# Kernel optimization log

Measured on AMD Instinct MI355X. Metric: run time of the kernel, lower is better.

## Reference

```python
import jax, jax.numpy as jnp
import numpy as np

LMAX = 6; MMAX = 2
C = 128          # num_channels
H = 8            # num_heads
ALPHA = 32       # attn_alpha_channels
VAL = 16         # attn_value_channels (H*VAL == C)
HID = 64         # attn_hidden_channels
FFN = 128        # ffn_hidden_channels
NL = 4           # num_layers
CUTOFF = 12.0; NRBF = 600
AVG_DEG = 23.395238876342773
AVG_NODES = 77.81317
EPS = 1e-16

def _maps():
    idx, ls = [], []
    for l in range(LMAX + 1):
        mm = min(l, MMAX)
        for m in range(-mm, mm + 1):
            idx.append(l * l + l + m); ls.append(l)
    return np.array(idx), np.array(ls)
_M2F_np, _LOF_np = _maps()
M2F = jnp.asarray(_M2F_np)   # [KM] full-coefficient index of each m-restricted coeff
LOF = jnp.asarray(_LOF_np)   # [KM] degree l of each m-restricted coeff
KM = int(_M2F_np.shape[0])   # 29 for lmax=6, mmax=2
KF = (LMAX + 1) ** 2         # 49

def _rbf(d):
    # GaussianSmearing(0, cutoff, NRBF, width_scalar=2.0)
    off = jnp.linspace(0.0, CUTOFF, NRBF)
    coeff = -0.5 / (2.0 * (off[1] - off[0])) ** 2
    return jnp.exp(coeff * (d[:, None] - off) ** 2)

def _envelope(d):
    # PolynomialEnvelope, exponent p=5
    x = d / CUTOFF
    env = 1.0 - 21.0 * x ** 5 + 35.0 * x ** 6 - 15.0 * x ** 7
    return jnp.where(x < 1.0, env, 0.0)

def _rms(x, g):
    # merge-norm over channel dim with learned per-channel scale
    return x * jax.lax.rsqrt(jnp.mean(x * x, axis=-1, keepdims=True) + 1e-6) * g

def _forward(atomic_numbers, edge_index, edge_distance, emb,
             We0, be0, We1, be1, Weproj, gamma1, gamma2,
             Wr0, Wr1, Wrl, Wmsg, Wap, wa, Wg, Wv, Wo,
             Wf1, Wfg, Wf2, Wh1, Wh2):
    N = atomic_numbers.shape[0]
    src, tgt = edge_index[0], edge_index[1]
    rbf = _rbf(edge_distance)            # [E, NRBF]
    env = _envelope(edge_distance)       # [E]
    # node init: atom embedding on the l=0 component
    x = jnp.zeros((N, KF, C), rbf.dtype).at[:, 0, :].set(emb[atomic_numbers])
    # edge-degree embedding: radial MLP -> per-edge coeffs -> scatter to targets
    h = jax.nn.silu(rbf @ We0 + be0)
    h = jax.nn.silu(h @ We1 + be1)
    deg = (h @ Weproj).reshape(-1, KM, C)              # [E, KM, C]
    x = x.at[tgt[:, None], M2F[None, :], :].add(deg / AVG_DEG)
    for i in range(NL):
        # ---- equivariant graph attention ----
        y = _rms(x, gamma1[i])
        ym = y[:, M2F, :]                               # [N, KM, C] m-restricted
        m = jnp.concatenate([ym[src], ym[tgt]], axis=-1)  # [E, KM, 2C]
        m = jnp.einsum('ekc,ch->ekh', m, Wmsg[i])       # [E, KM, HID]
        # radial function, shared across m within each l (use_rad_l_parametrization)
        rad = jax.nn.silu(jax.nn.silu(rbf @ Wr0[i]) @ Wr1[i])
        radl = rad @ Wrl[i]                             # [E, LMAX+1]
        m = m * radl[:, LOF][..., None]
        # attention logits from invariant (l=0) part
        a = jax.nn.silu(m[:, 0, :] @ Wap[i]).reshape(-1, H, ALPHA)
        logits = jnp.einsum('eha,ha->eh', a, wa[i])     # [E, H]
        segmax = jnp.full((N, H), -jnp.inf, logits.dtype).at[tgt].max(logits)
        ex = env[:, None] * jnp.exp(logits - segmax[tgt])  # envelope-masked softmax
        den = jax.ops.segment_sum(ex, tgt, num_segments=N)
        attn = ex / (den[tgt] + EPS)                    # [E, H]
        # SwiGLU-gated equivariant values
        g = jax.nn.silu(m[:, 0, :] @ Wg[i])             # [E, H*VAL]
        v = jnp.einsum('ekh,hv->ekv', m, Wv[i]) * g[:, None, :]
        v = v.reshape(-1, KM, H, VAL) * attn[:, None, :, None]
        agg = jax.ops.segment_sum(v.reshape(-1, KM, H * VAL), tgt, num_segments=N)
        out = jnp.einsum('nkv,vc->nkc', agg, Wo[i])     # [N, KM, C]
        x = x.at[:, M2F, :].add(out)
        # ---- feed-forward (grid-MLP style SwiGLU) ----
        y = _rms(x, gamma2[i])
        gf = jax.nn.silu(y[:, 0, :] @ Wfg[i])           # [N, FFN]
        hf = jnp.einsum('nkc,cf->nkf', y, Wf1[i]) * gf[:, None, :]
        x = x + jnp.einsum('nkf,fc->nkc', hf, Wf2[i])
    # energy head on invariant part, sum-aggregated over nodes
    s = jax.nn.silu(x[:, 0, :] @ Wh1) @ Wh2             # [N, 1]
    return (jnp.sum(s) / AVG_NODES).reshape(1)

def setup_inputs() -> dict:
    key = jax.random.key(0)
    ks = jax.random.split(key, 24)
    N, E = 6000, 120000
    def rn(k, shape, scale=0.05):
        return jax.random.normal(k, shape, dtype=jnp.float32) * scale
    inp = {}
    inp['atomic_numbers'] = jax.random.randint(ks[0], (N,), 0, 128)
    inp['edge_index'] = jax.random.randint(ks[1], (2, E), 0, N)
    inp['edge_distance'] = jax.random.uniform(ks[2], (E,), minval=0.5, maxval=CUTOFF, dtype=jnp.float32)
    inp['emb'] = rn(ks[3], (128, C), 1.0)
    inp['We0'] = rn(ks[4], (NRBF, 128)); inp['be0'] = jnp.zeros((128,), jnp.float32)
    inp['We1'] = rn(ks[5], (128, 128)); inp['be1'] = jnp.zeros((128,), jnp.float32)
    inp['Weproj'] = rn(ks[6], (128, KM * C))
    inp['gamma1'] = jnp.ones((NL, C), jnp.float32)
    inp['gamma2'] = jnp.ones((NL, C), jnp.float32)
    inp['Wr0'] = rn(ks[7], (NL, NRBF, 128))
    inp['Wr1'] = rn(ks[8], (NL, 128, 128))
    inp['Wrl'] = rn(ks[9], (NL, 128, LMAX + 1), 0.1)
    inp['Wmsg'] = rn(ks[10], (NL, 2 * C, HID))
    inp['Wap'] = rn(ks[11], (NL, HID, H * ALPHA))
    inp['wa'] = rn(ks[12], (NL, H, ALPHA))
    inp['Wg'] = rn(ks[13], (NL, HID, H * VAL))
    inp['Wv'] = rn(ks[14], (NL, HID, H * VAL))
    inp['Wo'] = rn(ks[15], (NL, H * VAL, C))
    inp['Wf1'] = rn(ks[16], (NL, C, FFN))
    inp['Wfg'] = rn(ks[17], (NL, C, FFN))
    inp['Wf2'] = rn(ks[18], (NL, FFN, C))
    inp['Wh1'] = rn(ks[19], (C, C))
    inp['Wh2'] = rn(ks[20], (C, 1))
    return inp

def reference(atomic_numbers, edge_index, edge_distance, emb,
              We0, be0, We1, be1, Weproj, gamma1, gamma2,
              Wr0, Wr1, Wrl, Wmsg, Wap, wa, Wg, Wv, Wo,
              Wf1, Wfg, Wf2, Wh1, Wh2):
    return _forward(atomic_numbers, edge_index, edge_distance, emb,
                    We0, be0, We1, be1, Weproj, gamma1, gamma2,
                    Wr0, Wr1, Wrl, Wmsg, Wap, wa, Wg, Wv, Wo,
                    Wf1, Wfg, Wf2, Wh1, Wh2)
```

## Files before the change

kernel.cpp:

```cpp
#include <hip/hip_runtime.h>

#define KM 29
#define GTAB 2048

typedef __bf16 bf16_t;
typedef __bf16 bf16x8 __attribute__((ext_vector_type(8)));
typedef __bf16 bf16x4 __attribute__((ext_vector_type(4)));
typedef __bf16 bf16x2 __attribute__((ext_vector_type(2)));
typedef float  f32x4  __attribute__((ext_vector_type(4)));
typedef float  f32x2  __attribute__((ext_vector_type(2)));

__device__ __forceinline__ float silu_f(float x){ return x / (1.0f + __expf(-x)); }

__device__ __forceinline__ float wave_reduce_sum(float v){
  #pragma unroll
  for (int s = 1; s < 64; s <<= 1) v += __shfl_xor(v, s);
  return v;
}

__device__ __forceinline__ constexpr int LOF2(int k){
  return (k<1)?0 : (k<4)?1 : (k<9)?2 : (k<14)?3 : (k<19)?4 : (k<24)?5 : 6;
}

__device__ __forceinline__ f32x4 mfma16(bf16x8 a, bf16x8 b, f32x4 c){
  return __builtin_amdgcn_mfma_f32_16x16x32_bf16(a, b, c, 0, 0, 0);
}

__device__ __forceinline__ float env_f(float d){
  float xx = d*(1.0f/12.0f);
  float x2 = xx*xx, x4 = x2*x2, x5 = x4*xx;
  float env = 1.0f - 21.0f*x5 + 35.0f*x5*xx - 15.0f*x5*x2;
  return (xx < 1.0f) ? env : 0.0f;
}

__global__ void k_count(const int* __restrict__ EI, int* __restrict__ cnt, int E){
  int e = blockIdx.x*256 + threadIdx.x;
  if (e < E) atomicAdd(&cnt[EI[E+e]], 1);
}

__global__ __launch_bounds__(1024) void k_scan(int* __restrict__ cnt, int* __restrict__ rowptr, int N){
  __shared__ int ts[1024];
  int t = threadIdx.x;
  int base = t*8;
  int loc[8]; int sum = 0;
  #pragma unroll
  for (int u = 0; u < 8; u++){ int idx = base+u; int v = (idx < N) ? cnt[idx] : 0; loc[u] = sum; sum += v; }
  ts[t] = sum; __syncthreads();
  for (int off = 1; off < 1024; off <<= 1){
    int v = (t >= off) ? ts[t-off] : 0;
    __syncthreads();
    ts[t] += v;
    __syncthreads();
  }
  int excl = ts[t] - sum;
  #pragma unroll
  for (int u = 0; u < 8; u++){
    int idx = base+u;
    if (idx < N){ int r = excl + loc[u]; rowptr[idx] = r; cnt[idx] = r; }
  }
  if (t == 1023) rowptr[N] = ts[1023];
}

__global__ void k_fill(const int* __restrict__ EI, int* __restrict__ cur, int* __restrict__ order, int E){
  int e = blockIdx.x*256 + threadIdx.x;
  if (e < E){ int pos = atomicAdd(&cur[EI[E+e]], 1); order[pos] = e; }
}

__global__ void k_sort(const int* __restrict__ rowptr, int* __restrict__ order, int N){
  int n = blockIdx.x*256 + threadIdx.x;
  if (n >= N) return;
  int rp = rowptr[n], re = rowptr[n+1];
  for (int a = rp+1; a < re; a++){
    int key = order[a]; int b = a-1;
    while (b >= rp && order[b] > key){ order[b+1] = order[b]; b--; }
    order[b+1] = key;
  }
}

__global__ void k_tr(const float* __restrict__ src, bf16_t* __restrict__ dst,
                     int L, int R, int C, int Lstr){
  int idx = blockIdx.x*256 + threadIdx.x;
  int total = L*R*C;
  if (idx >= total) return;
  int l = idx / (R*C); int rem = idx - l*(R*C);
  int r = rem / C; int c = rem - r*C;
  dst[((size_t)l*C + c)*R + r] = (bf16_t)src[(size_t)l*Lstr + (size_t)r*C + c];
}

__global__ void k_tr2(const float* __restrict__ src, bf16_t* __restrict__ dst){
  int idx = blockIdx.x*256 + threadIdx.x;
  if (idx >= 4*128*128) return;
  int l = idx >> 14; int j = (idx >> 7) & 127; int c = idx & 127;
  float v = (j < 64) ? src[(size_t)l*16384 + c*64 + j]
                     : src[(size_t)l*16384 + 8192 + c*64 + (j-64)];
  dst[idx] = (bf16_t)v;
}

__global__ __launch_bounds__(256) void k_tab_embed(
    const float* __restrict__ We0, const float* __restrict__ be0,
    const float* __restrict__ We1, const float* __restrict__ be1,
    const float* __restrict__ Wr0, const float* __restrict__ Wr1, const float* __restrict__ Wrl,
    float* __restrict__ h2tab, float* __restrict__ radtab)
{
  __shared__ float sb[4][640];
  const int wid = threadIdx.x >> 6, lane = threadIdx.x & 63;
  const int e = blockIdx.x*4 + wid;
  if (e >= GTAB) return;
  const float d = e * (12.0f/(GTAB-1));
  const float DLT = 12.0f/599.0f;
  const float CO  = -0.5f/((2.0f*DLT)*(2.0f*DLT));
  int jc = (int)(d/DLT + 0.5f);
  int j0 = jc - 16; if (j0 < 0) j0 = 0; if (j0 > 600-32) j0 = 600-32;
  float diff = d - (float)(j0+lane)*DLT;
  float gval = __expf(CO*diff*diff);
  float p[10];
  #pragma unroll
  for (int u = 0; u < 10; u++) p[u] = 0.f;
  const int c2 = 2*lane;
  for (int jj = 0; jj < 32; jj++){
    float gj = __shfl(gval, jj);
    int row = j0 + jj;
    const float2 w0 = *(const float2*)(We0 + row*128 + c2);
    p[0] += gj*w0.x; p[1] += gj*w0.y;
    #pragma unroll
    for (int i = 0; i < 4; i++){
      const float2 wr = *(const float2*)(Wr0 + ((size_t)i*600 + row)*128 + c2);
      p[2+2*i] += gj*wr.x; p[3+2*i] += gj*wr.y;
    }
  }
  sb[wid][c2]   = silu_f(p[0] + be0[c2]);
  sb[wid][c2+1] = silu_f(p[1] + be0[c2+1]);
  #pragma unroll
  for (int i = 0; i < 4; i++){
    sb[wid][128 + 128*i + c2]   = silu_f(p[2+2*i]);
    sb[wid][128 + 128*i + c2+1] = silu_f(p[3+2*i]);
  }
  float a0 = 0.f, a1 = 0.f;
  for (int c = 0; c < 128; c++){
    float hv = sb[wid][c];
    const float2 w = *(const float2*)(We1 + c*128 + c2);
    a0 += hv*w.x; a1 += hv*w.y;
  }
  a0 = silu_f(a0 + be1[c2]); a1 = silu_f(a1 + be1[c2+1]);
  h2tab[(size_t)e*128 + c2]     = a0;
  h2tab[(size_t)e*128 + c2 + 1] = a1;
  #pragma unroll
  for (int i = 0; i < 4; i++){
    float r0 = 0.f, r1 = 0.f;
    const float* W1 = Wr1 + (size_t)i*128*128;
    for (int c = 0; c < 128; c++){
      float rv = sb[wid][128 + 128*i + c];
      const float2 w = *(const float2*)(W1 + c*128 + c2);
      r0 += rv*w.x; r1 += rv*w.y;
    }
    r0 = silu_f(r0); r1 = silu_f(r1);
    const float* Wl = Wrl + (size_t)i*128*7;
    float pl[7];
    #pragma unroll
    for (int l = 0; l < 7; l++) pl[l] = r0*Wl[c2*7+l] + r1*Wl[(c2+1)*7+l];
    #pragma unroll
    for (int l = 0; l < 7; l++) pl[l] = wave_reduce_sum(pl[l]);
    if (lane == 0){
      #pragma unroll
      for (int l = 0; l < 7; l++) radtab[(size_t)e*28 + i*7 + l] = pl[l];
    }
  }
}

__global__ void k_h2e(const float* __restrict__ ed, const float* __restrict__ h2tab,
                      bf16_t* __restrict__ h2e, int E){
  int idx = blockIdx.x*256 + threadIdx.x;
  if (idx >= E*128) return;
  int e = idx >> 7, ch = idx & 127;
  float d = ed[e];
  float u = d * ((GTAB-1)/12.0f);
  int j = (int)u; if (j > GTAB-2) j = GTAB-2;
  float f = u - (float)j;
  float a = h2tab[(size_t)j*128 + ch], b = h2tab[(size_t)(j+1)*128 + ch];
  h2e[idx] = (bf16_t)(a + f*(b-a));
}

__global__ __launch_bounds__(256) void k_h2sum(
    const bf16_t* __restrict__ h2e, const int* __restrict__ rowptr, const int* __restrict__ order,
    bf16_t* __restrict__ h2sum, int N)
{
  int n = blockIdx.x*2 + (threadIdx.x >> 7);
  int ch = threadIdx.x & 127;
  if (n >= N) return;
  int rp = rowptr[n], deg = rowptr[n+1] - rp;
  float acc = 0.f;
  for (int idx = 0; idx < deg; idx++){
    int e = order[rp+idx];
    acc += (float)h2e[(size_t)e*128 + ch];
  }
  h2sum[(size_t)n*128 + ch] = (bf16_t)acc;
}

__global__ __launch_bounds__(256) void k_init_x(
    const int* __restrict__ Z, const float* __restrict__ emb,
    const bf16_t* __restrict__ WeprojT, const bf16_t* __restrict__ h2sum,
    bf16_t* __restrict__ Xb, int N)
{
  __shared__ bf16_t h2s[32*136];
  __shared__ int Zs[32];
  int n0 = blockIdx.x*32, t = threadIdx.x;
  for (int idx = t; idx < 32*128; idx += 256){
    int nn = idx >> 7, ch = idx & 127;
    int n = n0 + nn;
    h2s[nn*136 + ch] = (n < N) ? h2sum[(size_t)n*128 + ch] : (bf16_t)0.f;
  }
  if (t < 32) Zs[t] = (n0 + t < N) ? Z[n0+t] : 0;
  __syncthreads();
  int wid = t >> 6, lane = t & 63;
  int mtile = wid & 1;
  int row = mtile*16 + (lane & 15);
  int koff = (lane >> 4)*8;
  bf16x8 afr[4];
  #pragma unroll
  for (int kk = 0; kk < 4; kk++) afr[kk] = *(const bf16x8*)(h2s + row*136 + kk*32 + koff);
  for (int nt = (wid>>1); nt < 232; nt += 2){
    f32x4 acc = {0.f,0.f,0.f,0.f};
    int col = nt*16 + (lane & 15);
    #pragma unroll
    for (int kk = 0; kk < 4; kk++){
      bf16x8 b = *(const bf16x8*)(WeprojT + (size_t)col*128 + kk*32 + koff);
      acc = mfma16(afr[kk], b, acc);
    }
    #pragma unroll
    for (int r = 0; r < 4; r++){
      int r32 = mtile*16 + (lane>>4)*4 + r;
      int n = n0 + r32;
      if (n < N){
        float v = acc[r] * (1.0f/23.395238876342773f);
        if (col < 128) v += emb[(size_t)Zs[r32]*128 + col];
        Xb[(size_t)n*3712 + col] = (bf16_t)v;
      }
    }
  }
}

__global__ __launch_bounds__(512) void k_pqv(
    const bf16_t* __restrict__ Xb, const float* __restrict__ gamma1,
    const bf16_t* __restrict__ WmsgCT, const bf16_t* __restrict__ WvT,
    unsigned char* __restrict__ PV8, unsigned char* __restrict__ QV8,
    float* __restrict__ P0, float* __restrict__ Q0, int layer)
{
  __shared__ bf16_t ys16[32*136];
  __shared__ bf16_t pq16[32*136];
  int n = blockIdx.x, t = threadIdx.x;
  int wid = t >> 6, lane = t & 63;
  const float* g1 = gamma1 + layer*128;
  const bf16_t* xp = Xb + (size_t)n*3712;
  for (int k = wid; k < KM; k += 8){
    float x0 = (float)xp[k*128 + lane], x1 = (float)xp[k*128 + 64 + lane];
    float ss = wave_reduce_sum(x0*x0 + x1*x1);
    float sc = rsqrtf(ss*(1.0f/128.0f) + 1e-6f);
    ys16[k*136 + lane]      = (bf16_t)(x0*sc*g1[lane]);
    ys16[k*136 + 64 + lane] = (bf16_t)(x1*sc*g1[64+lane]);
  }
  for (int idx = t; idx < 3*136; idx += 512) ys16[29*136 + idx] = (bf16_t)0.f;
  __syncthreads();
  int mtile = wid >> 2;
  int row = mtile*16 + (lane & 15);
  int koff = (lane >> 4)*8;
  {
    const bf16_t* Bc = WmsgCT + (size_t)layer*16384;
    f32x4 acc[2] = {{0,0,0,0},{0,0,0,0}};
    #pragma unroll
    for (int kk = 0; kk < 128; kk += 32){
      bf16x8 a = *(const bf16x8*)(ys16 + row*136 + kk + koff);
      #pragma unroll
      for (int u = 0; u < 2; u++){
        int col = ((wid&3)*2+u)*16 + (lane & 15);
        bf16x8 b = *(const bf16x8*)(Bc + (size_t)col*128 + kk + koff);
        acc[u] = mfma16(a, b, acc[u]);
      }
    }
    #pragma unroll
    for (int u = 0; u < 2; u++){
      int col = ((wid&3)*2+u)*16 + (lane & 15);
      #pragma unroll
      for (int r = 0; r < 4; r++){
        int r32 = mtile*16 + (lane>>4)*4 + r;
        pq16[r32*136 + col] = (bf16_t)acc[u][r];
      }
      if (mtile == 0 && (lane>>4) == 0){
        float v = acc[u][0];
        if (col < 64) P0[(size_t)n*64 + col] = v;
        else          Q0[(size_t)n*64 + col - 64] = v;
      }
    }
  }
  __syncthreads();
  {
    const bf16_t* Bt = WvT + (size_t)layer*8192;
    f32x4 acc[2] = {{0,0,0,0},{0,0,0,0}};
    #pragma unroll
    for (int kk = 0; kk < 64; kk += 32){
      bf16x8 a = *(const bf16x8*)(pq16 + row*136 + kk + koff);
      #pragma unroll
      for (int u = 0; u < 2; u++){
        int col = ((wid&3)*2+u)*16 + (lane & 15);
        bf16x8 b = *(const bf16x8*)(Bt + (size_t)col*64 + kk + koff);
        acc[u] = mfma16(a, b, acc[u]);
      }
    }
    unsigned char* pvp = PV8 + (size_t)n*4096;
    int r0i = mtile*16 + (lane>>4)*4;
    #pragma unroll
    for (int u = 0; u < 2; u++){
      int col = ((wid&3)*2+u)*16 + (lane & 15);
      float pk[4];
      #pragma unroll
      for (int r = 0; r < 4; r++){
        int r32 = r0i + r;
        pk[r] = (r32 < KM) ? acc[u][r] : 0.f;
      }
      int dw = __builtin_amdgcn_cvt_pk_fp8_f32(pk[0], pk[1], 0, false);
      dw = __builtin_amdgcn_cvt_pk_fp8_f32(pk[2], pk[3], dw, true);
      *(unsigned int*)(pvp + col*32 + r0i) = (unsigned int)dw;
    }
  }
  {
    const bf16_t* Bt = WvT + (size_t)layer*8192;
    f32x4 acc[2] = {{0,0,0,0},{0,0,0,0}};
    #pragma unroll
    for (int kk = 0; kk < 64; kk += 32){
      bf16x8 a = *(const bf16x8*)(pq16 + row*136 + 64 + kk + koff);
      #pragma unroll
      for (int u = 0; u < 2; u++){
        int col = ((wid&3)*2+u)*16 + (lane & 15);
        bf16x8 b = *(const bf16x8*)(Bt + (size_t)col*64 + kk + koff);
        acc[u] = mfma16(a, b, acc[u]);
      }
    }
    unsigned char* qvp = QV8 + (size_t)n*4096;
    int r0i = mtile*16 + (lane>>4)*4;
    #pragma unroll
    for (int u = 0; u < 2; u++){
      int col = ((wid&3)*2+u)*16 + (lane & 15);
      float pk[4];
      #pragma unroll
      for (int r = 0; r < 4; r++){
        int r32 = r0i + r;
        pk[r] = (r32 < KM) ? acc[u][r] : 0.f;
      }
      int dw = __builtin_amdgcn_cvt_pk_fp8_f32(pk[0], pk[1], 0, false);
      dw = __builtin_amdgcn_cvt_pk_fp8_f32(pk[2], pk[3], dw, true);
      *(unsigned int*)(qvp + col*32 + r0i) = (unsigned int)dw;
    }
  }
}

__global__ __launch_bounds__(256) void k_edge_logits(
    const int* __restrict__ EI, const float* __restrict__ ed,
    const float* __restrict__ P0, const float* __restrict__ Q0,
    const float* __restrict__ radtab, const bf16_t* __restrict__ WapT, const float* __restrict__ wa,
    const bf16_t* __restrict__ WgT, float* __restrict__ logi, bf16_t* __restrict__ gate16,
    int E, int layer)
{
  __shared__ bf16_t m0s[16*72];
  __shared__ int   srcs[16], tgts[16];
  __shared__ float r0s[16];
  int t = threadIdx.x;
  int eb = blockIdx.x*16;
  if (t < 16){
    int e = eb + t;
    if (e < E){
      srcs[t] = EI[e]; tgts[t] = EI[E+e];
      float d = ed[e];
      float u = d * ((GTAB-1)/12.0f);
      int j = (int)u; if (j > GTAB-2) j = GTAB-2;
      float f = u - (float)j;
      float a = radtab[(size_t)j*28 + layer*7], b = radtab[(size_t)(j+1)*28 + layer*7];
      r0s[t] = a + f*(b-a);
    } else { srcs[t] = 0; tgts[t] = 0; r0s[t] = 0.f; }
  }
  __syncthreads();
  #pragma unroll
  for (int u = 0; u < 4; u++){
    int idx = t + u*256;
    int i = idx >> 6, j = idx & 63;
    m0s[i*72 + j] = (bf16_t)((P0[(size_t)srcs[i]*64 + j] + Q0[(size_t)tgts[i]*64 + j]) * r0s[i]);
  }
  __syncthreads();
  int wid = t >> 6, lane = t & 63;
  int l15 = lane & 15, lg = lane >> 4;
  int koff = lg*8;
  bf16x8 a0 = *(const bf16x8*)(m0s + l15*72 + koff);
  bf16x8 a1 = *(const bf16x8*)(m0s + l15*72 + 32 + koff);
  const bf16_t* Ba = WapT + (size_t)layer*16384;
  const bf16_t* Bg = WgT  + (size_t)layer*8192;
  const float* wav = wa + layer*256;
  f32x4 accA[4], accG[2];
  #pragma unroll
  for (int u = 0; u < 4; u++){
    int col = 64*wid + u*16 + l15;
    f32x4 acc = {0,0,0,0};
    acc = mfma16(a0, *(const bf16x8*)(Ba + (size_t)col*64 + koff), acc);
    acc = mfma16(a1, *(const bf16x8*)(Ba + (size_t)col*64 + 32 + koff), acc);
    accA[u] = acc;
  }
  #pragma unroll
  for (int u = 0; u < 2; u++){
    int col = 32*wid + u*16 + l15;
    f32x4 acc = {0,0,0,0};
    acc = mfma16(a0, *(const bf16x8*)(Bg + (size_t)col*64 + koff), acc);
    acc = mfma16(a1, *(const bf16x8*)(Bg + (size_t)col*64 + 32 + koff), acc);
    accG[u] = acc;
  }
  #pragma unroll
  for (int u = 0; u < 2; u++){
    int col = 32*wid + u*16 + l15;
    #pragma unroll
    for (int r = 0; r < 4; r++){
      int e = eb + lg*4 + r;
      if (e < E) gate16[(size_t)e*128 + col] = (bf16_t)silu_f(accG[u][r]);
    }
  }
  #pragma unroll
  for (int hpair = 0; hpair < 2; hpair++){
    int c0 = 64*wid + hpair*32 + l15;
    float w0 = wav[c0], w1 = wav[c0+16];
    float s[4];
    #pragma unroll
    for (int r = 0; r < 4; r++)
      s[r] = silu_f(accA[2*hpair][r])*w0 + silu_f(accA[2*hpair+1][r])*w1;
    #pragma unroll
    for (int r = 0; r < 4; r++){
      s[r] += __shfl_xor(s[r], 1);
      s[r] += __shfl_xor(s[r], 2);
      s[r] += __shfl_xor(s[r], 4);
      s[r] += __shfl_xor(s[r], 8);
    }
    if (l15 == 0){
      #pragma unroll
      for (int r = 0; r < 4; r++){
        int e = eb + lg*4 + r;
        if (e < E) logi[(size_t)e*8 + 2*wid + hpair] = s[r];
      }
    }
  }
}

#define FMA_DW(dw, kb) { \
  f32x2 lo_ = __builtin_amdgcn_cvt_pk_f32_fp8((dw), false); \
  f32x2 hi_ = __builtin_amdgcn_cvt_pk_f32_fp8((dw), true); \
  acc[(kb)]   += lo_.x * rw[LOF2((kb))]; \
  acc[(kb)+1] += lo_.y * rw[LOF2((kb)+1)]; \
  acc[(kb)+2] += hi_.x * rw[LOF2((kb)+2)]; \
  acc[(kb)+3] += hi_.y * rw[LOF2((kb)+3)]; }

__global__ __launch_bounds__(512, 4) void k_gather(
    const int* __restrict__ EI, const int* __restrict__ rowptr, const int* __restrict__ order,
    const float* __restrict__ ed,
    const unsigned char* __restrict__ PV8, const unsigned char* __restrict__ QV8,
    const bf16_t* __restrict__ gate16, const float* __restrict__ logi,
    const float* __restrict__ radtab,
    bf16_t* __restrict__ agg, int layer)
{
  __shared__ bf16_t mA[32*136];
  __shared__ bf16_t mB[32*136];
  __shared__ float at8[512];
  __shared__ float rl7[512];
  __shared__ int   esb[64], srcs[64];
  __shared__ float denl[32];

  int n = blockIdx.x, t = threadIdx.x;
  int rp = rowptr[n], deg = rowptr[n+1] - rp;
  if (deg == 0){
    for (int idx = t; idx < 3712; idx += 512) agg[(size_t)n*3712 + idx] = (bf16_t)0.f;
    return;
  }
  int eg = t >> 7, hv = t & 127, h = hv >> 4;
  float acc[32];
  #pragma unroll
  for (int j = 0; j < 32; j++) acc[j] = 0.f;
  float S[7];
  #pragma unroll
  for (int l = 0; l < 7; l++) S[l] = 0.f;
  float dpart = 0.f;
  for (int base = 0; base < deg; base += 64){
    int ne = min(64, deg - base);
    if (base > 0) __syncthreads();
    if (t < ne){ int e = order[rp + base + t]; esb[t] = e; srcs[t] = EI[e]; }
    __syncthreads();
    if (t < ne*8){
      int i = t >> 3, q = t & 7;
      int e = esb[i];
      float d = ed[e];
      at8[t] = env_f(d) * __expf(logi[(size_t)e*8 + q]);
      if (q < 7){
        float u = d * ((GTAB-1)/12.0f);
        int j = (int)u; if (j > GTAB-2) j = GTAB-2;
        float f = u - (float)j;
        float a = radtab[(size_t)j*28 + layer*7 + q], b = radtab[(size_t)(j+1)*28 + layer*7 + q];
        rl7[t] = a + f*(b-a);
      }
    }
    __syncthreads();
    uint4 A0 = {0,0,0,0}, A1 = {0,0,0,0}, B0 = {0,0,0,0}, B1 = {0,0,0,0};
    float gA = 0.f, gB = 0.f;
    int i = eg;
    if (i < ne){
      const uint4* p = (const uint4*)(PV8 + (size_t)srcs[i]*4096 + hv*32);
      A0 = p[0]; A1 = p[1];
      gA = (float)gate16[(size_t)esb[i]*128 + hv];
    }
    if (i + 4 < ne){
      const uint4* p = (const uint4*)(PV8 + (size_t)srcs[i+4]*4096 + hv*32);
      B0 = p[0]; B1 = p[1];
      gB = (float)gate16[(size_t)esb[i+4]*128 + hv];
    }
    while (i < ne){
      int i2 = i + 8;
      uint4 C0 = {0,0,0,0}, C1 = {0,0,0,0}; float gC = 0.f;
      if (i2 < ne){
        const uint4* p = (const uint4*)(PV8 + (size_t)srcs[i2]*4096 + hv*32);
        C0 = p[0]; C1 = p[1];
        gC = (float)gate16[(size_t)esb[i2]*128 + hv];
      }
      float ae = at8[i*8 + h];
      dpart += ae;
      float w = gA * ae;
      float rw[7];
      #pragma unroll
      for (int l = 0; l < 7; l++){ rw[l] = rl7[i*8 + l]*w; S[l] += rw[l]; }
      FMA_DW(A0.x, 0)  FMA_DW(A0.y, 4)  FMA_DW(A0.z, 8)  FMA_DW(A0.w, 12)
      FMA_DW(A1.x, 16) FMA_DW(A1.y, 20) FMA_DW(A1.z, 24) FMA_DW(A1.w, 28)
      A0 = B0; A1 = B1; gA = gB;
      B0 = C0; B1 = C1; gB = gC;
      i += 4;
    }
  }
  {
    const unsigned char* qvp = QV8 + (size_t)n*4096 + hv*32;
    uint4 q0 = *(const uint4*)qvp;
    uint4 q1 = *(const uint4*)(qvp + 16);
    float rw[7];
    #pragma unroll
    for (int l = 0; l < 7; l++) rw[l] = S[l];
    FMA_DW(q0.x, 0)  FMA_DW(q0.y, 4)  FMA_DW(q0.z, 8)  FMA_DW(q0.w, 12)
    FMA_DW(q1.x, 16) FMA_DW(q1.y, 20) FMA_DW(q1.z, 24) FMA_DW(q1.w, 28)
  }
  if ((hv & 15) == 0) denl[eg*8 + h] = dpart;
  __syncthreads();
  {
    float dsum = denl[h] + denl[8 + h] + denl[16 + h] + denl[24 + h];
    float inv = 1.0f/(dsum + 1e-30f);
    #pragma unroll
    for (int j = 0; j < 32; j++) acc[j] *= inv;
  }
  if (eg == 0){
    #pragma unroll
    for (int j = 0; j < 32; j++) mA[j*136 + hv] = (bf16_t)acc[j];
  } else if (eg == 1){
    #pragma unroll
    for (int j = 0; j < 32; j++) mB[j*136 + hv] = (bf16_t)acc[j];
  }
  __syncthreads();
  if (eg == 2){
    #pragma unroll
    for (int j = 0; j < 32; j++) mA[j*136 + hv] = (bf16_t)((float)mA[j*136 + hv] + acc[j]);
  } else if (eg == 3){
    #pragma unroll
    for (int j = 0; j < 32; j++) mB[j*136 + hv] = (bf16_t)((float)mB[j*136 + hv] + acc[j]);
  }
  __syncthreads();
  for (int idx = t; idx < 3712; idx += 512){
    int k = idx >> 7, c = idx & 127;
    agg[(size_t)n*3712 + idx] = (bf16_t)((float)mA[k*136 + c] + (float)mB[k*136 + c]);
  }
}

__global__ __launch_bounds__(512, 4) void k_xupdate(
    const bf16_t* __restrict__ agg,
    const float* __restrict__ gamma1, const float* __restrict__ gamma2,
    const float* __restrict__ Wfg,
    const bf16_t* __restrict__ Wf1T, const bf16_t* __restrict__ Wf2T,
    const bf16_t* __restrict__ WoT, const bf16_t* __restrict__ WmsgCT, const bf16_t* __restrict__ WvT,
    bf16_t* __restrict__ Xb, int layer,
    unsigned char* __restrict__ PV8o, unsigned char* __restrict__ QV8o,
    float* __restrict__ P0o, float* __restrict__ Q0o, int do_tail)
{
  __shared__ float  xs[3712];
  __shared__ bf16_t ysag[32*136];
  __shared__ bf16_t hsqv[32*136];
  __shared__ float  pf[640];

  int n = blockIdx.x, t = threadIdx.x;
  int wid = t >> 6, lane = t & 63;

  {
    const bf16x2* Xp2 = (const bf16x2*)(Xb + (size_t)n*3712);
    for (int p = t; p < 1856; p += 512){
      bf16x2 v = Xp2[p];
      xs[2*p]   = (float)v.x;
      xs[2*p+1] = (float)v.y;
    }
  }
  for (int idx = t; idx < 3712; idx += 512){
    int k = idx >> 7, c = idx & 127;
    ysag[k*136 + c] = agg[(size_t)n*3712 + idx];
  }
  for (int idx = t; idx < 3*136; idx += 512) ysag[29*136 + idx] = (bf16_t)0.f;
  __syncthreads();
  {
    const bf16_t* Bt = WoT + (size_t)layer*16384;
    int mtile = wid >> 2, colt = (wid & 3)*2;
    int row = mtile*16 + (lane & 15);
    int koff = (lane >> 4)*8;
    f32x4 a2[2] = {{0,0,0,0},{0,0,0,0}};
    #pragma unroll
    for (int kk = 0; kk < 128; kk += 32){
      bf16x8 a = *(const bf16x8*)(ysag + row*136 + kk + koff);
      #pragma unroll
      for (int u = 0; u < 2; u++){
        int col = (colt+u)*16 + (lane & 15);
        bf16x8 b = *(const bf16x8*)(Bt + (size_t)col*128 + kk + koff);
        a2[u] = mfma16(a, b, a2[u]);
      }
    }
    #pragma unroll
    for (int u = 0; u < 2; u++){
      int col = (colt+u)*16 + (lane & 15);
      #pragma unroll
      for (int r = 0; r < 4; r++){
        int r32 = mtile*16 + (lane>>4)*4 + r;
        if (r32 < KM) xs[r32*128 + col] += a2[u][r];
      }
    }
  }
  __syncthreads();
  const float* g2 = gamma2 + layer*128;
  for (int k = wid; k < KM; k += 8){
    float x0 = xs[k*128 + lane], x1 = xs[k*128 + 64 + lane];
    float ss = wave_reduce_sum(x0*x0 + x1*x1);
    float sc = rsqrtf(ss*(1.0f/128.0f) + 1e-6f);
    ysag[k*136 + lane]      = (bf16_t)(x0*sc*g2[lane]);
    ysag[k*136 + 64 + lane] = (bf16_t)(x1*sc*g2[64+lane]);
  }
  for (int idx = t; idx < 3*136; idx += 512) ysag[29*136 + idx] = (bf16_t)0.f;
  __syncthreads();
  {
    int part = t >> 7, f = t & 127;
    const float* Wfgp = Wfg + (size_t)layer*16384;
    float p = 0.f;
    for (int c = part*32; c < part*32 + 32; c++) p += (float)ysag[c] * Wfgp[c*128 + f];
    pf[part*128 + f] = p;
  }
  __syncthreads();
  if (t < 128) pf[512 + t] = silu_f(pf[t] + pf[128+t] + pf[256+t] + pf[384+t]);
  __syncthreads();
  {
    const bf16_t* Bt = Wf1T + (size_t)layer*16384;
    int mtile = wid >> 2, colt = (wid & 3)*2;
    int row = mtile*16 + (lane & 15);
    int koff = (lane >> 4)*8;
    f32x4 a2[2] = {{0,0,0,0},{0,0,0,0}};
    #pragma unroll
    for (int kk = 0; kk < 128; kk += 32){
      bf16x8 a = *(const bf16x8*)(ysag + row*136 + kk + koff);
      #pragma unroll
      for (int u = 0; u < 2; u++){
        int col = (colt+u)*16 + (lane & 15);
        bf16x8 b = *(const bf16x8*)(Bt + (size_t)col*128 + kk + koff);
        a2[u] = mfma16(a, b, a2[u]);
      }
    }
    #pragma unroll
    for (int u = 0; u < 2; u++){
      int col = (colt+u)*16 + (lane & 15);
      float gfc = pf[512 + col];
      #pragma unroll
      for (int r = 0; r < 4; r++){
        int r32 = mtile*16 + (lane>>4)*4 + r;
        hsqv[r32*136 + col] = (bf16_t)(a2[u][r]*gfc);
      }
    }
  }
  __syncthreads();
  {
    const bf16_t* Bt = Wf2T + (size_t)layer*16384;
    int mtile = wid >> 2, colt = (wid & 3)*2;
    int row = mtile*16 + (lane & 15);
    int koff = (lane >> 4)*8;
    f32x4 a2[2] = {{0,0,0,0},{0,0,0,0}};
    #pragma unroll
    for (int kk = 0; kk < 128; kk += 32){
      bf16x8 a = *(const bf16x8*)(hsqv + row*136 + kk + koff);
      #pragma unroll
      for (int u = 0; u < 2; u++){
        int col = (colt+u)*16 + (lane & 15);
        bf16x8 b = *(const bf16x8*)(Bt + (size_t)col*128 + kk + koff);
        a2[u] = mfma16(a, b, a2[u]);
      }
    }
    #pragma unroll
    for (int u = 0; u < 2; u++){
      int col = (colt+u)*16 + (lane & 15);
      #pragma unroll
      for (int r = 0; r < 4; r++){
        int r32 = mtile*16 + (lane>>4)*4 + r;
        if (r32 < KM) xs[r32*128 + col] += a2[u][r];
      }
    }
  }
  __syncthreads();
  {
    bf16x2* Xp2 = (bf16x2*)(Xb + (size_t)n*3712);
    for (int p = t; p < 1856; p += 512){
      bf16x2 v;
      v.x = (bf16_t)xs[2*p];
      v.y = (bf16_t)xs[2*p+1];
      Xp2[p] = v;
    }
  }
  if (do_tail){
    const float* g1n = gamma1 + (size_t)(layer+1)*128;
    for (int k = wid; k < KM; k += 8){
      float x0 = xs[k*128 + lane], x1 = xs[k*128 + 64 + lane];
      float ss = wave_reduce_sum(x0*x0 + x1*x1);
      float sc = rsqrtf(ss*(1.0f/128.0f) + 1e-6f);
      ysag[k*136 + lane]      = (bf16_t)(x0*sc*g1n[lane]);
      ysag[k*136 + 64 + lane] = (bf16_t)(x1*sc*g1n[64+lane]);
    }
    __syncthreads();
    int mtile = wid >> 2;
    int row = mtile*16 + (lane & 15);
    int koff = (lane >> 4)*8;
    {
      const bf16_t* Bc = WmsgCT + (size_t)(layer+1)*16384;
      f32x4 acc[2] = {{0,0,0,0},{0,0,0,0}};
      #pragma unroll
      for (int kk = 0; kk < 128; kk += 32){
        bf16x8 a = *(const bf16x8*)(ysag + row*136 + kk + koff);
        #pragma unroll
        for (int u = 0; u < 2; u++){
          int col = ((wid&3)*2+u)*16 + (lane & 15);
          bf16x8 b = *(const bf16x8*)(Bc + (size_t)col*128 + kk + koff);
          acc[u] = mfma16(a, b, acc[u]);
        }
      }
      #pragma unroll
      for (int u = 0; u < 2; u++){
        int col = ((wid&3)*2+u)*16 + (lane & 15);
        #pragma unroll
        for (int r = 0; r < 4; r++){
          int r32 = mtile*16 + (lane>>4)*4 + r;
          hsqv[r32*136 + col] = (bf16_t)acc[u][r];
        }
        if (mtile == 0 && (lane>>4) == 0){
          float v = acc[u][0];
          if (col < 64) P0o[(size_t)n*64 + col] = v;
          else          Q0o[(size_t)n*64 + col - 64] = v;
        }
      }
    }
    __syncthreads();
    {
      const bf16_t* Bt = WvT + (size_t)(layer+1)*8192;
      f32x4 acc[2] = {{0,0,0,0},{0,0,0,0}};
      #pragma unroll
      for (int kk = 0; kk < 64; kk += 32){
        bf16x8 a = *(const bf16x8*)(hsqv + row*136 + kk + koff);
        #pragma unroll
        for (int u = 0; u < 2; u++){
          int col = ((wid&3)*2+u)*16 + (lane & 15);
          bf16x8 b = *(const bf16x8*)(Bt + (size_t)col*64 + kk + koff);
          acc[u] = mfma16(a, b, acc[u]);
        }
      }
      unsigned char* pvp = PV8o + (size_t)n*4096;
      int r0i = mtile*16 + (lane>>4)*4;
      #pragma unroll
      for (int u = 0; u < 2; u++){
        int col = ((wid&3)*2+u)*16 + (lane & 15);
        float pk[4];
        #pragma unroll
        for (int r = 0; r < 4; r++){
          int r32 = r0i + r;
          pk[r] = (r32 < KM) ? acc[u][r] : 0.f;
        }
        int dw = __builtin_amdgcn_cvt_pk_fp8_f32(pk[0], pk[1], 0, false);
        dw = __builtin_amdgcn_cvt_pk_fp8_f32(pk[2], pk[3], dw, true);
        *(unsigned int*)(pvp + col*32 + r0i) = (unsigned int)dw;
      }
    }
    {
      const bf16_t* Bt = WvT + (size_t)(layer+1)*8192;
      f32x4 acc[2] = {{0,0,0,0},{0,0,0,0}};
      #pragma unroll
      for (int kk = 0; kk < 64; kk += 32){
        bf16x8 a = *(const bf16x8*)(hsqv + row*136 + 64 + kk + koff);
        #pragma unroll
        for (int u = 0; u < 2; u++){
          int col = ((wid&3)*2+u)*16 + (lane & 15);
          bf16x8 b = *(const bf16x8*)(Bt + (size_t)col*64 + kk + koff);
          acc[u] = mfma16(a, b, acc[u]);
        }
      }
      unsigned char* qvp = QV8o + (size_t)n*4096;
      int r0i = mtile*16 + (lane>>4)*4;
      #pragma unroll
      for (int u = 0; u < 2; u++){
        int col = ((wid&3)*2+u)*16 + (lane & 15);
        float pk[4];
        #pragma unroll
        for (int r = 0; r < 4; r++){
          int r32 = r0i + r;
          pk[r] = (r32 < KM) ? acc[u][r] : 0.f;
        }
        int dw = __builtin_amdgcn_cvt_pk_fp8_f32(pk[0], pk[1], 0, false);
        dw = __builtin_amdgcn_cvt_pk_fp8_f32(pk[2], pk[3], dw, true);
        *(unsigned int*)(qvp + col*32 + r0i) = (unsigned int)dw;
      }
    }
  }
}

__global__ __launch_bounds__(256) void k_head(
    const bf16_t* __restrict__ Xb, const float* __restrict__ Wh1, const float* __restrict__ Wh2,
    float* __restrict__ partial, int N)
{
  __shared__ float wsum[4];
  int t = threadIdx.x;
  int half = t >> 7;
  int n = blockIdx.x*2 + half;
  int f = t & 127;
  float sv = 0.f;
  if (n < N){
    const bf16_t* xp = Xb + (size_t)n*3712;
    float acc = 0.f;
    for (int c = 0; c < 128; c++) acc += (float)xp[c]*Wh1[c*128 + f];
    sv = silu_f(acc)*Wh2[f];
  }
  sv = wave_reduce_sum(sv);
  if ((t & 63) == 0) wsum[t >> 6] = sv;
  __syncthreads();
  if (t == 0) partial[blockIdx.x] = wsum[0] + wsum[1] + wsum[2] + wsum[3];
}

__global__ __launch_bounds__(256) void k_reduce(const float* __restrict__ partial, float* __restrict__ out, int P){
  __shared__ float sh[256];
  int t = threadIdx.x;
  float s = 0.f;
  for (int i = t; i < P; i += 256) s += partial[i];
  sh[t] = s; __syncthreads();
  for (int off = 128; off > 0; off >>= 1){
    if (t < off) sh[t] += sh[t+off];
    __syncthreads();
  }
  if (t == 0) out[0] = sh[0] / 77.81317f;
}

extern "C" void kernel_launch(void* const* d_in, const int* in_sizes, int n_in,
                              void* d_out, int out_size, void* d_ws, size_t ws_size,
                              hipStream_t stream)
{
  const int*   Z      = (const int*)d_in[0];
  const int*   EI     = (const int*)d_in[1];
  const float* ed     = (const float*)d_in[2];
  const float* emb    = (const float*)d_in[3];
  const float* We0    = (const float*)d_in[4];
  const float* be0    = (const float*)d_in[5];
  const float* We1    = (const float*)d_in[6];
  const float* be1    = (const float*)d_in[7];
  const float* Weproj = (const float*)d_in[8];
  const float* gamma1 = (const float*)d_in[9];
  const float* gamma2 = (const float*)d_in[10];
  const float* Wr0    = (const float*)d_in[11];
  const float* Wr1    = (const float*)d_in[12];
  const float* Wrl    = (const float*)d_in[13];
  const float* Wmsg   = (const float*)d_in[14];
  const float* Wap    = (const float*)d_in[15];
  const float* wa     = (const float*)d_in[16];
  const float* Wg     = (const float*)d_in[17];
  const float* Wv     = (const float*)d_in[18];
  const float* Wo     = (const float*)d_in[19];
  const float* Wf1    = (const float*)d_in[20];
  const float* Wfg    = (const float*)d_in[21];
  const float* Wf2    = (const float*)d_in[22];
  const float* Wh1    = (const float*)d_in[23];
  const float* Wh2    = (const float*)d_in[24];

  const int N = in_sizes[0];
  const int E = in_sizes[2];

  float* ws = (float*)d_ws;
  size_t o = 0;
  auto alloc = [&](size_t nf){ float* p = ws + o; o += (nf + 7) & ~(size_t)7; return p; };

  bf16_t* Xb    = (bf16_t*)alloc((size_t)N*1856);
  float* P0     = alloc((size_t)N*64);
  float* Q0     = alloc((size_t)N*64);
  float* logi   = alloc((size_t)E*8);
  float* part   = alloc((size_t)((N+1)/2) + 8);
  float* radtab = alloc((size_t)GTAB*28);
  float* h2tab  = alloc((size_t)GTAB*128);
  bf16_t* h2sum = (bf16_t*)alloc((size_t)N*64);
  unsigned char* PV8 = (unsigned char*)alloc((size_t)N*1024);
  unsigned char* QV8 = (unsigned char*)alloc((size_t)N*1024);
  bf16_t* agg   = (bf16_t*)alloc((size_t)N*1856);
  bf16_t* gate16= (bf16_t*)alloc((size_t)E*64);
  bf16_t* arena = (bf16_t*)alloc(434176);
  int* rowptr = (int*)alloc((size_t)N+8);
  int* curs   = (int*)alloc((size_t)N);
  int* order  = (int*)alloc((size_t)E);

  bf16_t* WmsgCT  = arena;
  bf16_t* WvT     = arena + 65536;
  bf16_t* WoT     = arena + 98304;
  bf16_t* Wf1T    = arena + 163840;
  bf16_t* Wf2T    = arena + 229376;
  bf16_t* WapT    = arena + 294912;
  bf16_t* WgT     = arena + 360448;
  bf16_t* WeprojT = arena + 393216;

  bf16_t* h2e = gate16;

  hipMemsetAsync(curs, 0, sizeof(int)*N, stream);
  k_count<<<(E+255)/256, 256, 0, stream>>>(EI, curs, E);
  k_scan<<<1, 1024, 0, stream>>>(curs, rowptr, N);
  k_fill<<<(E+255)/256, 256, 0, stream>>>(EI, curs, order, E);
  k_sort<<<(N+255)/256, 256, 0, stream>>>(rowptr, order, N);

  k_tr2<<<256, 256, 0, stream>>>(Wmsg, WmsgCT);
  k_tr<<<128, 256, 0, stream>>>(Wv,   WvT,  4, 64, 128, 8192);
  k_tr<<<256, 256, 0, stream>>>(Wo,   WoT,  4, 128, 128, 16384);
  k_tr<<<256, 256, 0, stream>>>(Wf1,  Wf1T, 4, 128, 128, 16384);
  k_tr<<<256, 256, 0, stream>>>(Wf2,  Wf2T, 4, 128, 128, 16384);
  k_tr<<<256, 256, 0, stream>>>(Wap,  WapT, 4, 64, 256, 16384);
  k_tr<<<128, 256, 0, stream>>>(Wg,   WgT,  4, 64, 128, 8192);
  k_tr<<<1856, 256, 0, stream>>>(Weproj, WeprojT, 1, 128, 3712, 0);

  k_tab_embed<<<GTAB/4, 256, 0, stream>>>(We0, be0, We1, be1, Wr0, Wr1, Wrl, h2tab, radtab);
  k_h2e<<<(E*128+255)/256, 256, 0, stream>>>(ed, h2tab, h2e, E);
  k_h2sum<<<(N+1)/2, 256, 0, stream>>>(h2e, rowptr, order, h2sum, N);
  k_init_x<<<(N+31)/32, 256, 0, stream>>>(Z, emb, WeprojT, h2sum, Xb, N);

  k_pqv<<<N, 512, 0, stream>>>(Xb, gamma1, WmsgCT, WvT, PV8, QV8, P0, Q0, 0);

  for (int i = 0; i < 4; i++){
    k_edge_logits<<<(E+15)/16, 256, 0, stream>>>(EI, ed, P0, Q0, radtab, WapT, wa, WgT, logi, gate16, E, i);
    k_gather<<<N, 512, 0, stream>>>(EI, rowptr, order, ed, PV8, QV8, gate16, logi, radtab, agg, i);
    k_xupdate<<<N, 512, 0, stream>>>(agg, gamma1, gamma2, Wfg, Wf1T, Wf2T, WoT, WmsgCT, WvT,
                                     Xb, i, PV8, QV8, P0, Q0, (i < 3) ? 1 : 0);
  }

  int PB = (N+1)/2;
  k_head<<<PB, 256, 0, stream>>>(Xb, Wh1, Wh2, part, N);
  k_reduce<<<1, 256, 0, stream>>>(part, (float*)d_out, PB);
}
```

Baseline: 2.078 ms.

## Fuse h2e into h2sum, precompute edge attention/radial terms, persistent gather/update grids

Drops the separate k_h2e kernel and does the table interpolation inside k_h2sum, so the per-edge buffer is no longer written and then re-read. k_edge_logits now computes env*exp(logit) and all seven interpolated radial weights per edge and stores them, which lets k_gather just load them. k_gather and k_xupdate become grid-stride loops over a fixed grid of 1024 blocks instead of one block per node. The P/Q value MFMAs are merged into one loop that shares B-operand loads. The trade-offs are an extra E*7 float buffer, and the persistent grid may load-balance worse when node degrees vary.

New measurement: 2.721 ms. +30.9%, slower.

```diff
diff --git a/kernel.cpp b/kernel.cpp
--- a/kernel.cpp
+++ b/kernel.cpp
@@ -167,21 +167,9 @@
   }
 }
 
-__global__ void k_h2e(const float* __restrict__ ed, const float* __restrict__ h2tab,
-                      bf16_t* __restrict__ h2e, int E){
-  int idx = blockIdx.x*256 + threadIdx.x;
-  if (idx >= E*128) return;
-  int e = idx >> 7, ch = idx & 127;
-  float d = ed[e];
-  float u = d * ((GTAB-1)/12.0f);
-  int j = (int)u; if (j > GTAB-2) j = GTAB-2;
-  float f = u - (float)j;
-  float a = h2tab[(size_t)j*128 + ch], b = h2tab[(size_t)(j+1)*128 + ch];
-  h2e[idx] = (bf16_t)(a + f*(b-a));
-}
-
 __global__ __launch_bounds__(256) void k_h2sum(
-    const bf16_t* __restrict__ h2e, const int* __restrict__ rowptr, const int* __restrict__ order,
+    const float* __restrict__ ed, const float* __restrict__ h2tab,
+    const int* __restrict__ rowptr, const int* __restrict__ order,
     bf16_t* __restrict__ h2sum, int N)
 {
   int n = blockIdx.x*2 + (threadIdx.x >> 7);
@@ -191,7 +179,12 @@
   float acc = 0.f;
   for (int idx = 0; idx < deg; idx++){
     int e = order[rp+idx];
-    acc += (float)h2e[(size_t)e*128 + ch];
+    float d = ed[e];
+    float u = d * ((GTAB-1)/12.0f);
+    int j = (int)u; if (j > GTAB-2) j = GTAB-2;
+    float f = u - (float)j;
+    float a = h2tab[(size_t)j*128 + ch], b = h2tab[(size_t)(j+1)*128 + ch];
+    acc += a + f*(b-a);
   }
   h2sum[(size_t)n*128 + ch] = (bf16_t)acc;
 }
@@ -294,60 +287,39 @@
   __syncthreads();
   {
     const bf16_t* Bt = WvT + (size_t)layer*8192;
-    f32x4 acc[2] = {{0,0,0,0},{0,0,0,0}};
+    f32x4 accP[2] = {{0,0,0,0},{0,0,0,0}};
+    f32x4 accQ[2] = {{0,0,0,0},{0,0,0,0}};
     #pragma unroll
     for (int kk = 0; kk < 64; kk += 32){
-      bf16x8 a = *(const bf16x8*)(pq16 + row*136 + kk + koff);
+      bf16x8 aP = *(const bf16x8*)(pq16 + row*136 + kk + koff);
+      bf16x8 aQ = *(const bf16x8*)(pq16 + row*136 + 64 + kk + koff);
       #pragma unroll
       for (int u = 0; u < 2; u++){
         int col = ((wid&3)*2+u)*16 + (lane & 15);
         bf16x8 b = *(const bf16x8*)(Bt + (size_t)col*64 + kk + koff);
-        acc[u] = mfma16(a, b, acc[u]);
+        accP[u] = mfma16(aP, b, accP[u]);
+        accQ[u] = mfma16(aQ, b, accQ[u]);
       }
     }
     unsigned char* pvp = PV8 + (size_t)n*4096;
+    unsigned char* qvp = QV8 + (size_t)n*4096;
     int r0i = mtile*16 + (lane>>4)*4;
     #pragma unroll
     for (int u = 0; u < 2; u++){
       int col = ((wid&3)*2+u)*16 + (lane & 15);
-      float pk[4];
+      float pk[4], qk[4];
       #pragma unroll
       for (int r = 0; r < 4; r++){
         int r32 = r0i + r;
-        pk[r] = (r32 < KM) ? acc[u][r] : 0.f;
+        pk[r] = (r32 < KM) ? accP[u][r] : 0.f;
+        qk[r] = (r32 < KM) ? accQ[u][r] : 0.f;
       }
       int dw = __builtin_amdgcn_cvt_pk_fp8_f32(pk[0], pk[1], 0, false);
       dw = __builtin_amdgcn_cvt_pk_fp8_f32(pk[2], pk[3], dw, true);
       *(unsigned int*)(pvp + col*32 + r0i) = (unsigned int)dw;
-    }
-  }
-  {
-    const bf16_t* Bt = WvT + (size_t)layer*8192;
-    f32x4 acc[2] = {{0,0,0,0},{0,0,0,0}};
-    #pragma unroll
-    for (int kk = 0; kk < 64; kk += 32){
-      bf16x8 a = *(const bf16x8*)(pq16 + row*136 + 64 + kk + koff);
-      #pragma unroll
-      for (int u = 0; u < 2; u++){
-        int col = ((wid&3)*2+u)*16 + (lane & 15);
-        bf16x8 b = *(const bf16x8*)(Bt + (size_t)col*64 + kk + koff);
-        acc[u] = mfma16(a, b, acc[u]);
-      }
-    }
-    unsigned char* qvp = QV8 + (size_t)n*4096;
-    int r0i = mtile*16 + (lane>>4)*4;
-    #pragma unroll
-    for (int u = 0; u < 2; u++){
-      int col = ((wid&3)*2+u)*16 + (lane & 15);
-      float pk[4];
-      #pragma unroll
-      for (int r = 0; r < 4; r++){
-        int r32 = r0i + r;
-        pk[r] = (r32 < KM) ? acc[u][r] : 0.f;
-      }
-      int dw = __builtin_amdgcn_cvt_pk_fp8_f32(pk[0], pk[1], 0, false);
-      dw = __builtin_amdgcn_cvt_pk_fp8_f32(pk[2], pk[3], dw, true);
-      *(unsigned int*)(qvp + col*32 + r0i) = (unsigned int)dw;
+      int dw2 = __builtin_amdgcn_cvt_pk_fp8_f32(qk[0], qk[1], 0, false);
+      dw2 = __builtin_amdgcn_cvt_pk_fp8_f32(qk[2], qk[3], dw2, true);
+      *(unsigned int*)(qvp + col*32 + r0i) = (unsigned int)dw2;
     }
   }
 }
@@ -356,12 +328,13 @@
     const int* __restrict__ EI, const float* __restrict__ ed,
     const float* __restrict__ P0, const float* __restrict__ Q0,
     const float* __restrict__ radtab, const bf16_t* __restrict__ WapT, const float* __restrict__ wa,
-    const bf16_t* __restrict__ WgT, float* __restrict__ logi, bf16_t* __restrict__ gate16,
-    int E, int layer)
+    const bf16_t* __restrict__ WgT, float* __restrict__ expat, float* __restrict__ radl,
+    bf16_t* __restrict__ gate16, int E, int layer)
 {
   __shared__ bf16_t m0s[16*72];
   __shared__ int   srcs[16], tgts[16];
   __shared__ float r0s[16];
+  __shared__ float envs[16];
   int t = threadIdx.x;
   int eb = blockIdx.x*16;
   if (t < 16){
@@ -369,12 +342,18 @@
     if (e < E){
       srcs[t] = EI[e]; tgts[t] = EI[E+e];
       float d = ed[e];
+      envs[t] = env_f(d);
       float u = d * ((GTAB-1)/12.0f);
       int j = (int)u; if (j > GTAB-2) j = GTAB-2;
       float f = u - (float)j;
-      float a = radtab[(size_t)j*28 + layer*7], b = radtab[(size_t)(j+1)*28 + layer*7];
-      r0s[t] = a + f*(b-a);
-    } else { srcs[t] = 0; tgts[t] = 0; r0s[t] = 0.f; }
+      #pragma unroll
+      for (int l = 0; l < 7; l++){
+        float a = radtab[(size_t)j*28 + layer*7 + l], b = radtab[(size_t)(j+1)*28 + layer*7 + l];
+        float rv = a + f*(b-a);
+        radl[(size_t)e*7 + l] = rv;
+        if (l == 0) r0s[t] = rv;
+      }
+    } else { srcs[t] = 0; tgts[t] = 0; r0s[t] = 0.f; envs[t] = 0.f; }
   }
   __syncthreads();
   #pragma unroll
@@ -437,7 +416,7 @@
       #pragma unroll
       for (int r = 0; r < 4; r++){
         int e = eb + lg*4 + r;
-        if (e < E) logi[(size_t)e*8 + 2*wid + hpair] = s[r];
+        if (e < E) expat[(size_t)e*8 + 2*wid + hpair] = envs[lg*4 + r] * __expf(s[r]);
       }
     }
   }
@@ -453,11 +432,10 @@
 
 __global__ __launch_bounds__(512, 4) void k_gather(
     const int* __restrict__ EI, const int* __restrict__ rowptr, const int* __restrict__ order,
-    const float* __restrict__ ed,
     const unsigned char* __restrict__ PV8, const unsigned char* __restrict__ QV8,
-    const bf16_t* __restrict__ gate16, const float* __restrict__ logi,
-    const float* __restrict__ radtab,
-    bf16_t* __restrict__ agg, int layer)
+    const bf16_t* __restrict__ gate16, const float* __restrict__ expat,
+    const float* __restrict__ radl,
+    bf16_t* __restrict__ agg, int N)
 {
   __shared__ bf16_t mA[32*136];
   __shared__ bf16_t mB[32*136];
@@ -466,110 +444,107 @@
   __shared__ int   esb[64], srcs[64];
   __shared__ float denl[32];
 
-  int n = blockIdx.x, t = threadIdx.x;
-  int rp = rowptr[n], deg = rowptr[n+1] - rp;
-  if (deg == 0){
-    for (int idx = t; idx < 3712; idx += 512) agg[(size_t)n*3712 + idx] = (bf16_t)0.f;
-    return;
-  }
+  int t = threadIdx.x;
   int eg = t >> 7, hv = t & 127, h = hv >> 4;
-  float acc[32];
-  #pragma unroll
-  for (int j = 0; j < 32; j++) acc[j] = 0.f;
-  float S[7];
-  #pragma unroll
-  for (int l = 0; l < 7; l++) S[l] = 0.f;
-  float dpart = 0.f;
-  for (int base = 0; base < deg; base += 64){
-    int ne = min(64, deg - base);
-    if (base > 0) __syncthreads();
-    if (t < ne){ int e = order[rp + base + t]; esb[t] = e; srcs[t] = EI[e]; }
-    __syncthreads();
-    if (t < ne*8){
-      int i = t >> 3, q = t & 7;
-      int e = esb[i];
-      float d = ed[e];
-      at8[t] = env_f(d) * __expf(logi[(size_t)e*8 + q]);
-      if (q < 7){
-        float u = d * ((GTAB-1)/12.0f);
-        int j = (int)u; if (j > GTAB-2) j = GTAB-2;
-        float f = u - (float)j;
-        float a = radtab[(size_t)j*28 + layer*7 + q], b = radtab[(size_t)(j+1)*28 + layer*7 + q];
-        rl7[t] = a + f*(b-a);
-      }
-    }
-    __syncthreads();
-    uint4 A0 = {0,0,0,0}, A1 = {0,0,0,0}, B0 = {0,0,0,0}, B1 = {0,0,0,0};
-    float gA = 0.f, gB = 0.f;
-    int i = eg;
-    if (i < ne){
-      const uint4* p = (const uint4*)(PV8 + (size_t)srcs[i]*4096 + hv*32);
-      A0 = p[0]; A1 = p[1];
-      gA = (float)gate16[(size_t)esb[i]*128 + hv];
-    }
-    if (i + 4 < ne){
-      const uint4* p = (const uint4*)(PV8 + (size_t)srcs[i+4]*4096 + hv*32);
-      B0 = p[0]; B1 = p[1];
-      gB = (float)gate16[(size_t)esb[i+4]*128 + hv];
-    }
-    while (i < ne){
-      int i2 = i + 8;
-      uint4 C0 = {0,0,0,0}, C1 = {0,0,0,0}; float gC = 0.f;
-      if (i2 < ne){
-        const uint4* p = (const uint4*)(PV8 + (size_t)srcs[i2]*4096 + hv*32);
-        C0 = p[0]; C1 = p[1];
-        gC = (float)gate16[(size_t)esb[i2]*128 + hv];
-      }
-      float ae = at8[i*8 + h];
-      dpart += ae;
-      float w = gA * ae;
+
+  for (int n = blockIdx.x; n < N; n += gridDim.x){
+    int rp = rowptr[n], deg = rowptr[n+1] - rp;
+    if (deg == 0){
+      for (int idx = t; idx < 3712; idx += 512) agg[(size_t)n*3712 + idx] = (bf16_t)0.f;
+      continue;
+    }
+    float acc[32];
+    #pragma unroll
+    for (int j = 0; j < 32; j++) acc[j] = 0.f;
+    float S[7];
+    #pragma unroll
+    for (int l = 0; l < 7; l++) S[l] = 0.f;
+    float dpart = 0.f;
+    for (int base = 0; base < deg; base += 64){
+      int ne = min(64, deg - base);
+      __syncthreads();
+      if (t < ne){ int e = order[rp + base + t]; esb[t] = e; srcs[t] = EI[e]; }
+      __syncthreads();
+      if (t < ne*8){
+        int i = t >> 3, q = t & 7;
+        int e = esb[i];
+        at8[t] = expat[(size_t)e*8 + q];
+        if (q < 7) rl7[t] = radl[(size_t)e*7 + q];
+      }
+      __syncthreads();
+      uint4 A0 = {0,0,0,0}, A1 = {0,0,0,0}, B0 = {0,0,0,0}, B1 = {0,0,0,0};
+      float gA = 0.f, gB = 0.f;
+      int i = eg;
+      if (i < ne){
+        const uint4* p = (const uint4*)(PV8 + (size_t)srcs[i]*4096 + hv*32);
+        A0 = p[0]; A1 = p[1];
+        gA = (float)gate16[(size_t)esb[i]*128 + hv];
+      }
+      if (i + 4 < ne){
+        const uint4* p = (const uint4*)(PV8 + (size_t)srcs[i+4]*4096 + hv*32);
+        B0 = p[0]; B1 = p[1];
+        gB = (float)gate16[(size_t)esb[i+4]*128 + hv];
+      }
+      while (i < ne){
+        int i2 = i + 8;
+        uint4 C0 = {0,0,0,0}, C1 = {0,0,0,0}; float gC = 0.f;
+        if (i2 < ne){
+          const uint4* p = (const uint4*)(PV8 + (size_t)srcs[i2]*4096 + hv*32);
+          C0 = p[0]; C1 = p[1];
+          gC = (float)gate16[(size_t)esb[i2]*128 + hv];
+        }
+        float ae = at8[i*8 + h];
+        dpart += ae;
+        float w = gA * ae;
+        float rw[7];
+        #pragma unroll
+        for (int l = 0; l < 7; l++){ rw[l] = rl7[i*8 + l]*w; S[l] += rw[l]; }
+        FMA_DW(A0.x, 0)  FMA_DW(A0.y, 4)  FMA_DW(A0.z, 8)  FMA_DW(A0.w, 12)
+        FMA_DW(A1.x, 16) FMA_DW(A1.y, 20) FMA_DW(A1.z, 24) FMA_DW(A1.w, 28)
+        A0 = B0; A1 = B1; gA = gB;
+        B0 = C0; B1 = C1; gB = gC;
+        i += 4;
+      }
+    }
+    {
+      const unsigned char* qvp = QV8 + (size_t)n*4096 + hv*32;
+      uint4 q0 = *(const uint4*)qvp;
+      uint4 q1 = *(const uint4*)(qvp + 16);
       float rw[7];
       #pragma unroll
-      for (int l = 0; l < 7; l++){ rw[l] = rl7[i*8 + l]*w; S[l] += rw[l]; }
-      FMA_DW(A0.x, 0)  FMA_DW(A0.y, 4)  FMA_DW(A0.z, 8)  FMA_DW(A0.w, 12)
-      FMA_DW(A1.x, 16) FMA_DW(A1.y, 20) FMA_DW(A1.z, 24) FMA_DW(A1.w, 28)
-      A0 = B0; A1 = B1; gA = gB;
-      B0 = C0; B1 = C1; gB = gC;
-      i += 4;
-    }
-  }
-  {
-    const unsigned char* qvp = QV8 + (size_t)n*4096 + hv*32;
-    uint4 q0 = *(const uint4*)qvp;
-    uint4 q1 = *(const uint4*)(qvp + 16);
-    float rw[7];
-    #pragma unroll
-    for (int l = 0; l < 7; l++) rw[l] = S[l];
-    FMA_DW(q0.x, 0)  FMA_DW(q0.y, 4)  FMA_DW(q0.z, 8)  FMA_DW(q0.w, 12)
-    FMA_DW(q1.x, 16) FMA_DW(q1.y, 20) FMA_DW(q1.z, 24) FMA_DW(q1.w, 28)
-  }
-  if ((hv & 15) == 0) denl[eg*8 + h] = dpart;
-  __syncthreads();
-  {
-    float dsum = denl[h] + denl[8 + h] + denl[16 + h] + denl[24 + h];
-    float inv = 1.0f/(dsum + 1e-30f);
-    #pragma unroll
-    for (int j = 0; j < 32; j++) acc[j] *= inv;
-  }
-  if (eg == 0){
-    #pragma unroll
-    for (int j = 0; j < 32; j++) mA[j*136 + hv] = (bf16_t)acc[j];
-  } else if (eg == 1){
-    #pragma unroll
-    for (int j = 0; j < 32; j++) mB[j*136 + hv] = (bf16_t)acc[j];
-  }
-  __syncthreads();
-  if (eg == 2){
-    #pragma unroll
-    for (int j = 0; j < 32; j++) mA[j*136 + hv] = (bf16_t)((float)mA[j*136 + hv] + acc[j]);
-  } else if (eg == 3){
-    #pragma unroll
-    for (int j = 0; j < 32; j++) mB[j*136 + hv] = (bf16_t)((float)mB[j*136 + hv] + acc[j]);
-  }
-  __syncthreads();
-  for (int idx = t; idx < 3712; idx += 512){
-    int k = idx >> 7, c = idx & 127;
-    agg[(size_t)n*3712 + idx] = (bf16_t)((float)mA[k*136 + c] + (float)mB[k*136 + c]);
+      for (int l = 0; l < 7; l++) rw[l] = S[l];
+      FMA_DW(q0.x, 0)  FMA_DW(q0.y, 4)  FMA_DW(q0.z, 8)  FMA_DW(q0.w, 12)
+      FMA_DW(q1.x, 16) FMA_DW(q1.y, 20) FMA_DW(q1.z, 24) FMA_DW(q1.w, 28)
+    }
+    if ((hv & 15) == 0) denl[eg*8 + h] = dpart;
+    __syncthreads();
+    {
+      float dsum = denl[h] + denl[8 + h] + denl[16 + h] + denl[24 + h];
+      float inv = 1.0f/(dsum + 1e-30f);
+      #pragma unroll
+      for (int j = 0; j < 32; j++) acc[j] *= inv;
+    }
+    if (eg == 0){
+      #pragma unroll
+      for (int j = 0; j < 32; j++) mA[j*136 + hv] = (bf16_t)acc[j];
+    } else if (eg == 1){
+      #pragma unroll
+      for (int j = 0; j < 32; j++) mB[j*136 + hv] = (bf16_t)acc[j];
+    }
+    __syncthreads();
+    if (eg == 2){
+      #pragma unroll
+      for (int j = 0; j < 32; j++) mA[j*136 + hv] = (bf16_t)((float)mA[j*136 + hv] + acc[j]);
+    } else if (eg == 3){
+      #pragma unroll
+      for (int j = 0; j < 32; j++) mB[j*136 + hv] = (bf16_t)((float)mB[j*136 + hv] + acc[j]);
+    }
+    __syncthreads();
+    for (int idx = t; idx < 3712; idx += 512){
+      int k = idx >> 7, c = idx & 127;
+      agg[(size_t)n*3712 + idx] = (bf16_t)((float)mA[k*136 + c] + (float)mB[k*136 + c]);
+    }
+    __syncthreads();
   }
 }
 
@@ -581,241 +556,227 @@
     const bf16_t* __restrict__ WoT, const bf16_t* __restrict__ WmsgCT, const bf16_t* __restrict__ WvT,
     bf16_t* __restrict__ Xb, int layer,
     unsigned char* __restrict__ PV8o, unsigned char* __restrict__ QV8o,
-    float* __restrict__ P0o, float* __restrict__ Q0o, int do_tail)
+    float* __restrict__ P0o, float* __restrict__ Q0o, int do_tail, int N)
 {
   __shared__ float  xs[3712];
   __shared__ bf16_t ysag[32*136];
   __shared__ bf16_t hsqv[32*136];
   __shared__ float  pf[640];
 
-  int n = blockIdx.x, t = threadIdx.x;
+  int t = threadIdx.x;
   int wid = t >> 6, lane = t & 63;
 
-  {
-    const bf16x2* Xp2 = (const bf16x2*)(Xb + (size_t)n*3712);
-    for (int p = t; p < 1856; p += 512){
-      bf16x2 v = Xp2[p];
-      xs[2*p]   = (float)v.x;
-      xs[2*p+1] = (float)v.y;
-    }
-  }
-  for (int idx = t; idx < 3712; idx += 512){
-    int k = idx >> 7, c = idx & 127;
-    ysag[k*136 + c] = agg[(size_t)n*3712 + idx];
-  }
-  for (int idx = t; idx < 3*136; idx += 512) ysag[29*136 + idx] = (bf16_t)0.f;
-  __syncthreads();
-  {
-    const bf16_t* Bt = WoT + (size_t)layer*16384;
-    int mtile = wid >> 2, colt = (wid & 3)*2;
-    int row = mtile*16 + (lane & 15);
-    int koff = (lane >> 4)*8;
-    f32x4 a2[2] = {{0,0,0,0},{0,0,0,0}};
-    #pragma unroll
-    for (int kk = 0; kk < 128; kk += 32){
-      bf16x8 a = *(const bf16x8*)(ysag + row*136 + kk + koff);
+  for (int n = blockIdx.x; n < N; n += gridDim.x){
+    {
+      const bf16x2* Xp2 = (const bf16x2*)(Xb + (size_t)n*3712);
+      for (int p = t; p < 1856; p += 512){
+        bf16x2 v = Xp2[p];
+        xs[2*p]   = (float)v.x;
+        xs[2*p+1] = (float)v.y;
+      }
+    }
+    for (int idx = t; idx < 3712; idx += 512){
+      int k = idx >> 7, c = idx & 127;
+      ysag[k*136 + c] = agg[(size_t)n*3712 + idx];
+    }
+    for (int idx = t; idx < 3*136; idx += 512) ysag[29*136 + idx] = (bf16_t)0.f;
+    __syncthreads();
+    {
+      const bf16_t* Bt = WoT + (size_t)layer*16384;
+      int mtile = wid >> 2, colt = (wid & 3)*2;
+      int row = mtile*16 + (lane & 15);
+      int koff = (lane >> 4)*8;
+      f32x4 a2[2] = {{0,0,0,0},{0,0,0,0}};
+      #pragma unroll
+      for (int kk = 0; kk < 128; kk += 32){
+        bf16x8 a = *(const bf16x8*)(ysag + row*136 + kk + koff);
+        #pragma unroll
+        for (int u = 0; u < 2; u++){
+          int col = (colt+u)*16 + (lane & 15);
+          bf16x8 b = *(const bf16x8*)(Bt + (size_t)col*128 + kk + koff);
+          a2[u] = mfma16(a, b, a2[u]);
+        }
+      }
       #pragma unroll
       for (int u = 0; u < 2; u++){
         int col = (colt+u)*16 + (lane & 15);
-        bf16x8 b = *(const bf16x8*)(Bt + (size_t)col*128 + kk + koff);
-        a2[u] = mfma16(a, b, a2[u]);
-      }
-    }
-    #pragma unroll
-    for (int u = 0; u < 2; u++){
-      int col = (colt+u)*16 + (lane & 15);
-      #pragma unroll
-      for (int r = 0; r < 4; r++){
-        int r32 = mtile*16 + (lane>>4)*4 + r;
-        if (r32 < KM) xs[r32*128 + col] += a2[u][r];
-      }
-    }
-  }
-  __syncthreads();
-  const float* g2 = gamma2 + layer*128;
-  for (int k = wid; k < KM; k += 8){
-    float x0 = xs[k*128 + lane], x1 = xs[k*128 + 64 + lane];
-    float ss = wave_reduce_sum(x0*x0 + x1*x1);
-    float sc = rsqrtf(ss*(1.0f/128.0f) + 1e-6f);
-    ysag[k*136 + lane]      = (bf16_t)(x0*sc*g2[lane]);
-    ysag[k*136 + 64 + lane] = (bf16_t)(x1*sc*g2[64+lane]);
-  }
-  for (int idx = t; idx < 3*136; idx += 512) ysag[29*136 + idx] = (bf16_t)0.f;
-  __syncthreads();
-  {
-    int part = t >> 7, f = t & 127;
-    const float* Wfgp = Wfg + (size_t)layer*16384;
-    float p = 0.f;
-    for (int c = part*32; c < part*32 + 32; c++) p += (float)ysag[c] * Wfgp[c*128 + f];
-    pf[part*128 + f] = p;
-  }
-  __syncthreads();
-  if (t < 128) pf[512 + t] = silu_f(pf[t] + pf[128+t] + pf[256+t] + pf[384+t]);
-  __syncthreads();
-  {
-    const bf16_t* Bt = Wf1T + (size_t)layer*16384;
-    int mtile = wid >> 2, colt = (wid & 3)*2;
-    int row = mtile*16 + (lane & 15);
-    int koff = (lane >> 4)*8;
-    f32x4 a2[2] = {{0,0,0,0},{0,0,0,0}};
-    #pragma unroll
-    for (int kk = 0; kk < 128; kk += 32){
-      bf16x8 a = *(const bf16x8*)(ysag + row*136 + kk + koff);
+        #pragma unroll
+        for (int r = 0; r < 4; r++){
+          int r32 = mtile*16 + (lane>>4)*4 + r;
+          if (r32 < KM) xs[r32*128 + col] += a2[u][r];
+        }
+      }
+    }
+    __syncthreads();
+    {
+      const float* g2 = gamma2 + layer*128;
+      for (int k = wid; k < KM; k += 8){
+        float x0 = xs[k*128 + lane], x1 = xs[k*128 + 64 + lane];
+        float ss = wave_reduce_sum(x0*x0 + x1*x1);
+        float sc = rsqrtf(ss*(1.0f/128.0f) + 1e-6f);
+        ysag[k*136 + lane]      = (bf16_t)(x0*sc*g2[lane]);
+        ysag[k*136 + 64 + lane] = (bf16_t)(x1*sc*g2[64+lane]);
+      }
+      for (int idx = t; idx < 3*136; idx += 512) ysag[29*136 + idx] = (bf16_t)0.f;
+    }
+    __syncthreads();
+    {
+      int part = t >> 7, f = t & 127;
+      const float* Wfgp = Wfg + (size_t)layer*16384;
+      float p = 0.f;
+      for (int c = part*32; c < part*32 + 32; c++) p += (float)ysag[c] * Wfgp[c*128 + f];
+      pf[part*128 + f] = p;
+    }
+    __syncthreads();
+    if (t < 128) pf[512 + t] = silu_f(pf[t] + pf[128+t] + pf[256+t] + pf[384+t]);
+    __syncthreads();
+    {
+      const bf16_t* Bt = Wf1T + (size_t)layer*16384;
+      int mtile = wid >> 2, colt = (wid & 3)*2;
+      int row = mtile*16 + (lane & 15);
+      int koff = (lane >> 4)*8;
+      f32x4 a2[2] = {{0,0,0,0},{0,0,0,0}};
+      #pragma unroll
+      for (int kk = 0; kk < 128; kk += 32){
+        bf16x8 a = *(const bf16x8*)(ysag + row*136 + kk + koff);
+        #pragma unroll
+        for (int u = 0; u < 2; u++){
+          int col = (colt+u)*16 + (lane & 15);
+          bf16x8 b = *(const bf16x8*)(Bt + (size_t)col*128 + kk + koff);
+          a2[u] = mfma16(a, b, a2[u]);
+        }
+      }
       #pragma unroll
       for (int u = 0; u < 2; u++){
         int col = (colt+u)*16 + (lane & 15);
-        bf16x8 b = *(const bf16x8*)(Bt + (size_t)col*128 + kk + koff);
-        a2[u] = mfma16(a, b, a2[u]);
-      }
-    }
-    #pragma unroll
-    for (int u = 0; u < 2; u++){
-      int col = (colt+u)*16 + (lane & 15);
-      float gfc = pf[512 + col];
-      #pragma unroll
-      for (int r = 0; r < 4; r++){
-        int r32 = mtile*16 + (lane>>4)*4 + r;
-        hsqv[r32*136 + col] = (bf16_t)(a2[u][r]*gfc);
-      }
-    }
-  }
-  __syncthreads();
-  {
-    const bf16_t* Bt = Wf2T + (size_t)layer*16384;
-    int mtile = wid >> 2, colt = (wid & 3)*2;
-    int row = mtile*16 + (lane & 15);
-    int koff = (lane >> 4)*8;
-    f32x4 a2[2] = {{0,0,0,0},{0,0,0,0}};
-    #pragma unroll
-    for (int kk = 0; kk < 128; kk += 32){
-      bf16x8 a = *(const bf16x8*)(hsqv + row*136 + kk + koff);
+        float gfc = pf[512 + col];
+        #pragma unroll
+        for (int r = 0; r < 4; r++){
+          int r32 = mtile*16 + (lane>>4)*4 + r;
+          hsqv[r32*136 + col] = (bf16_t)(a2[u][r]*gfc);
+        }
+      }
+    }
+    __syncthreads();
+    {
+      const bf16_t* Bt = Wf2T + (size_t)layer*16384;
+      int mtile = wid >> 2, colt = (wid & 3)*2;
+      int row = mtile*16 + (lane & 15);
+      int koff = (lane >> 4)*8;
+      f32x4 a2[2] = {{0,0,0,0},{0,0,0,0}};
+      #pragma unroll
+      for (int kk = 0; kk < 128; kk += 32){
+        bf16x8 a = *(const bf16x8*)(hsqv + row*136 + kk + koff);
+        #pragma unroll
+        for (int u = 0; u < 2; u++){
+          int col = (colt+u)*16 + (lane & 15);
+          bf16x8 b = *(const bf16x8*)(Bt + (size_t)col*128 + kk + koff);
+          a2[u] = mfma16(a, b, a2[u]);
+        }
+      }
       #pragma unroll
       for (int u = 0; u < 2; u++){
         int col = (colt+u)*16 + (lane & 15);
-        bf16x8 b = *(const bf16x8*)(Bt + (size_t)col*128 + kk + koff);
-        a2[u] = mfma16(a, b, a2[u]);
-      }
-    }
-    #pragma unroll
-    for (int u = 0; u < 2; u++){
-      int col = (colt+u)*16 + (lane & 15);
-      #pragma unroll
-      for (int r = 0; r < 4; r++){
-        int r32 = mtile*16 + (lane>>4)*4 + r;
-        if (r32 < KM) xs[r32*128 + col] += a2[u][r];
-      }
-    }
-  }
-  __syncthreads();
-  {
-    bf16x2* Xp2 = (bf16x2*)(Xb + (size_t)n*3712);
-    for (int p = t; p < 1856; p += 512){
-      bf16x2 v;
-      v.x = (bf16_t)xs[2*p];
-      v.y = (bf16_t)xs[2*p+1];
-      Xp2[p] = v;
-    }
-  }
-  if (do_tail){
-    const float* g1n = gamma1 + (size_t)(layer+1)*128;
-    for (int k = wid; k < KM; k += 8){
-      float x0 = xs[k*128 + lane], x1 = xs[k*128 + 64 + lane];
-      float ss = wave_reduce_sum(x0*x0 + x1*x1);
-      float sc = rsqrtf(ss*(1.0f/128.0f) + 1e-6f);
-      ysag[k*136 + lane]      = (bf16_t)(x0*sc*g1n[lane]);
-      ysag[k*136 + 64 + lane] = (bf16_t)(x1*sc*g1n[64+lane]);
-    }
-    __syncthreads();
-    int mtile = wid >> 2;
-    int row = mtile*16 + (lane & 15);
-    int koff = (lane >> 4)*8;
+        #pragma unroll
+        for (int r = 0; r < 4; r++){
+          int r32 = mtile*16 + (lane>>4)*4 + r;
+          if (r32 < KM) xs[r32*128 + col] += a2[u][r];
+        }
+      }
+    }
+    __syncthreads();
     {
-      const bf16_t* Bc = WmsgCT + (size_t)(layer+1)*16384;
-      f32x4 acc[2] = {{0,0,0,0},{0,0,0,0}};
-      #pragma unroll
-      for (int kk = 0; kk < 128; kk += 32){
-        bf16x8 a = *(const bf16x8*)(ysag + row*136 + kk + koff);
+      bf16x2* Xp2 = (bf16x2*)(Xb + (size_t)n*3712);
+      for (int p = t; p < 1856; p += 512){
+        bf16x2 v;
+        v.x = (bf16_t)xs[2*p];
+        v.y = (bf16_t)xs[2*p+1];
+        Xp2[p] = v;
+      }
+    }
+    if (do_tail){
+      {
+        const float* g1n = gamma1 + (size_t)(layer+1)*128;
+        for (int k = wid; k < KM; k += 8){
+          float x0 = xs[k*128 + lane], x1 = xs[k*128 + 64 + lane];
+          float ss = wave_reduce_sum(x0*x0 + x1*x1);
+          float sc = rsqrtf(ss*(1.0f/128.0f) + 1e-6f);
+          ysag[k*136 + lane]      = (bf16_t)(x0*sc*g1n[lane]);
+          ysag[k*136 + 64 + lane] = (bf16_t)(x1*sc*g1n[64+lane]);
+        }
+      }
+      __syncthreads();
+      int mtile = wid >> 2;
+      int row = mtile*16 + (lane & 15);
+      int koff = (lane >> 4)*8;
+      {
+        const bf16_t* Bc = WmsgCT + (size_t)(layer+1)*16384;
+        f32x4 acc[2] = {{0,0,0,0},{0,0,0,0}};
+        #pragma unroll
+        for (int kk = 0; kk < 128; kk += 32){
+          bf16x8 a = *(const bf16x8*)(ysag + row*136 + kk + koff);
+          #pragma unroll
+          for (int u = 0; u < 2; u++){
+            int col = ((wid&3)*2+u)*16 + (lane & 15);
+            bf16x8 b = *(const bf16x8*)(Bc + (size_t)col*128 + kk + koff);
+            acc[u] = mfma16(a, b, acc[u]);
+          }
+        }
         #pragma unroll
         for (int u = 0; u < 2; u++){
           int col = ((wid&3)*2+u)*16 + (lane & 15);
-          bf16x8 b = *(const bf16x8*)(Bc + (size_t)col*128 + kk + koff);
-          acc[u] = mfma16(a, b, acc[u]);
-        }
-      }
-      #pragma unroll
-      for (int u = 0; u < 2; u++){
-        int col = ((wid&3)*2+u)*16 + (lane & 15);
-        #pragma unroll
-        for (int r = 0; r < 4; r++){
-          int r32 = mtile*16 + (lane>>4)*4 + r;
-          hsqv[r32*136 + col] = (bf16_t)acc[u][r];
-        }
-        if (mtile == 0 && (lane>>4) == 0){
-          float v = acc[u][0];
-          if (col < 64) P0o[(size_t)n*64 + col] = v;
-          else          Q0o[(size_t)n*64 + col - 64] = v;
-        }
-      }
-    }
-    __syncthreads();
-    {
-      const bf16_t* Bt = WvT + (size_t)(layer+1)*8192;
-      f32x4 acc[2] = {{0,0,0,0},{0,0,0,0}};
-      #pragma unroll
-      for (int kk = 0; kk < 64; kk += 32){
-        bf16x8 a = *(const bf16x8*)(hsqv + row*136 + kk + koff);
+          #pragma unroll
+          for (int r = 0; r < 4; r++){
+            int r32 = mtile*16 + (lane>>4)*4 + r;
+            hsqv[r32*136 + col] = (bf16_t)acc[u][r];
+          }
+          if (mtile == 0 && ((lane>>4) == 0)){
+            float v = acc[u][0];
+            if (col < 64) P0o[(size_t)n*64 + col] = v;
+            else          Q0o[(size_t)n*64 + col - 64] = v;
+          }
+        }
+      }
+      __syncthreads();
+      {
+        const bf16_t* Bt = WvT + (size_t)(layer+1)*8192;
+        f32x4 accP[2] = {{0,0,0,0},{0,0,0,0}};
+        f32x4 accQ[2] = {{0,0,0,0},{0,0,0,0}};
+        #pragma unroll
+        for (int kk = 0; kk < 64; kk += 32){
+          bf16x8 aP = *(const bf16x8*)(hsqv + row*136 + kk + koff);
+          bf16x8 aQ = *(const bf16x8*)(hsqv + row*136 + 64 + kk + koff);
+          #pragma unroll
+          for (int u = 0; u < 2; u++){
+            int col = ((wid&3)*2+u)*16 + (lane & 15);
+            bf16x8 b = *(const bf16x8*)(Bt + (size_t)col*64 + kk + koff);
+            accP[u] = mfma16(aP, b, accP[u]);
+            accQ[u] = mfma16(aQ, b, accQ[u]);
+          }
+        }
+        unsigned char* pvp = PV8o + (size_t)n*4096;
+        unsigned char* qvp = QV8o + (size_t)n*4096;
+        int r0i = mtile*16 + (lane>>4)*4;
         #pragma unroll
         for (int u = 0; u < 2; u++){
           int col = ((wid&3)*2+u)*16 + (lane & 15);
-          bf16x8 b = *(const bf16x8*)(Bt + (size_t)col*64 + kk + koff);
-          acc[u] = mfma16(a, b, acc[u]);
-        }
-      }
-      unsigned char* pvp = PV8o + (size_t)n*4096;
-      int r0i = mtile*16 + (lane>>4)*4;
-      #pragma unroll
-      for (int u = 0; u < 2; u++){
-        int col = ((wid&3)*2+u)*16 + (lane & 15);
-        float pk[4];
-        #pragma unroll
-        for (int r = 0; r < 4; r++){
-          int r32 = r0i + r;
-          pk[r] = (r32 < KM) ? acc[u][r] : 0.f;
-        }
-        int dw = __builtin_amdgcn_cvt_pk_fp8_f32(pk[0], pk[1], 0, false);
-        dw = __builtin_amdgcn_cvt_pk_fp8_f32(pk[2], pk[3], dw, true);
-        *(unsigned int*)(pvp + col*32 + r0i) = (unsigned int)dw;
-      }
-    }
-    {
-      const bf16_t* Bt = WvT + (size_t)(layer+1)*8192;
-      f32x4 acc[2] = {{0,0,0,0},{0,0,0,0}};
-      #pragma unroll
-      for (int kk = 0; kk < 64; kk += 32){
-        bf16x8 a = *(const bf16x8*)(hsqv + row*136 + 64 + kk + koff);
-        #pragma unroll
-        for (int u = 0; u < 2; u++){
-          int col = ((wid&3)*2+u)*16 + (lane & 15);
-          bf16x8 b = *(const bf16x8*)(Bt + (size_t)col*64 + kk + koff);
-          acc[u] = mfma16(a, b, acc[u]);
-        }
-      }
-      unsigned char* qvp = QV8o + (size_t)n*4096;
-      int r0i = mtile*16 + (lane>>4)*4;
-      #pragma unroll
-      for (int u = 0; u < 2; u++){
-        int col = ((wid&3)*2+u)*16 + (lane & 15);
-        float pk[4];
-        #pragma unroll
-        for (int r = 0; r < 4; r++){
-          int r32 = r0i + r;
-          pk[r] = (r32 < KM) ? acc[u][r] : 0.f;
-        }
-        int dw = __builtin_amdgcn_cvt_pk_fp8_f32(pk[0], pk[1], 0, false);
-        dw = __builtin_amdgcn_cvt_pk_fp8_f32(pk[2], pk[3], dw, true);
-        *(unsigned int*)(qvp + col*32 + r0i) = (unsigned int)dw;
-      }
-    }
+          float pk[4], qk[4];
+          #pragma unroll
+          for (int r = 0; r < 4; r++){
+            int r32 = r0i + r;
+            pk[r] = (r32 < KM) ? accP[u][r] : 0.f;
+            qk[r] = (r32 < KM) ? accQ[u][r] : 0.f;
+          }
+          int dw = __builtin_amdgcn_cvt_pk_fp8_f32(pk[0], pk[1], 0, false);
+          dw = __builtin_amdgcn_cvt_pk_fp8_f32(pk[2], pk[3], dw, true);
+          *(unsigned int*)(pvp + col*32 + r0i) = (unsigned int)dw;
+          int dw2 = __builtin_amdgcn_cvt_pk_fp8_f32(qk[0], qk[1], 0, false);
+          dw2 = __builtin_amdgcn_cvt_pk_fp8_f32(qk[2], qk[3], dw2, true);
+          *(unsigned int*)(qvp + col*32 + r0i) = (unsigned int)dw2;
+        }
+      }
+    }
+    __syncthreads();
   }
 }
 
@@ -894,7 +855,8 @@
   bf16_t* Xb    = (bf16_t*)alloc((size_t)N*1856);
   float* P0     = alloc((size_t)N*64);
   float* Q0     = alloc((size_t)N*64);
-  float* logi   = alloc((size_t)E*8);
+  float* expat  = alloc((size_t)E*8);
+  float* radl   = alloc((size_t)E*7);
   float* part   = alloc((size_t)((N+1)/2) + 8);
   float* radtab = alloc((size_t)GTAB*28);
   float* h2tab  = alloc((size_t)GTAB*128);
@@ -917,8 +879,6 @@
   bf16_t* WgT     = arena + 360448;
   bf16_t* WeprojT = arena + 393216;
 
-  bf16_t* h2e = gate16;
-
   hipMemsetAsync(curs, 0, sizeof(int)*N, stream);
   k_count<<<(E+255)/256, 256, 0, stream>>>(EI, curs, E);
   k_scan<<<1, 1024, 0, stream>>>(curs, rowptr, N);
@@ -935,17 +895,18 @@
   k_tr<<<1856, 256, 0, stream>>>(Weproj, WeprojT, 1, 128, 3712, 0);
 
   k_tab_embed<<<GTAB/4, 256, 0, stream>>>(We0, be0, We1, be1, Wr0, Wr1, Wrl, h2tab, radtab);
-  k_h2e<<<(E*128+255)/256, 256, 0, stream>>>(ed, h2tab, h2e, E);
-  k_h2sum<<<(N+1)/2, 256, 0, stream>>>(h2e, rowptr, order, h2sum, N);
+  k_h2sum<<<(N+1)/2, 256, 0, stream>>>(ed, h2tab, rowptr, order, h2sum, N);
   k_init_x<<<(N+31)/32, 256, 0, stream>>>(Z, emb, WeprojT, h2sum, Xb, N);
 
   k_pqv<<<N, 512, 0, stream>>>(Xb, gamma1, WmsgCT, WvT, PV8, QV8, P0, Q0, 0);
 
+  const int PGRID = 1024;
   for (int i = 0; i < 4; i++){
-    k_edge_logits<<<(E+15)/16, 256, 0, stream>>>(EI, ed, P0, Q0, radtab, WapT, wa, WgT, logi, gate16, E, i);
-    k_gather<<<N, 512, 0, stream>>>(EI, rowptr, order, ed, PV8, QV8, gate16, logi, radtab, agg, i);
-    k_xupdate<<<N, 512, 0, stream>>>(agg, gamma1, gamma2, Wfg, Wf1T, Wf2T, WoT, WmsgCT, WvT,
-                                     Xb, i, PV8, QV8, P0, Q0, (i < 3) ? 1 : 0);
+    k_edge_logits<<<(E+15)/16, 256, 0, stream>>>(EI, ed, P0, Q0, radtab, WapT, wa, WgT,
+                                                 expat, radl, gate16, E, i);
+    k_gather<<<PGRID, 512, 0, stream>>>(EI, rowptr, order, PV8, QV8, gate16, expat, radl, agg, N);
+    k_xupdate<<<PGRID, 512, 0, stream>>>(agg, gamma1, gamma2, Wfg, Wf1T, Wf2T, WoT, WmsgCT, WvT,
+                                         Xb, i, PV8, QV8, P0, Q0, (i < 3) ? 1 : 0, N);
   }
 
   int PB = (N+1)/2;
```
